# Kernel optimization log

Measured on AMD Instinct MI355X. Metric: run time of the kernel, lower is better.

Reference implementation:

```python
import jax, jax.numpy as jnp
import numpy as np

BATCH = 8192
EXP_DIM = 1024        # experience_dim
DICT_SIZE = 4096      # dictionary_size
SPARSITY = 0.1        # sparsity_level
REG = 0.1             # regularization_strength
STEP = 0.1            # ISTA step size (hardcoded in module)
N_ITERS = 20          # min(max_iterations, 20)
K_SPARSE = int(DICT_SIZE * SPARSITY)  # 409


def setup_inputs() -> dict:
    key = jax.random.key(0)
    k_x, k_dict = jax.random.split(key)
    experiences_batch = jax.random.normal(k_x, (BATCH, EXP_DIM), dtype=jnp.float32)
    # Dictionary init as in __init__: normal*0.1, then row-normalize atoms.
    raw = jax.random.normal(k_dict, (DICT_SIZE, EXP_DIM), dtype=jnp.float32) * 0.1
    atom_norms = jnp.linalg.norm(raw, axis=1, keepdims=True)
    dictionary = raw / (atom_norms + 1e-8)
    return {"experiences_batch": experiences_batch, "dictionary": dictionary}


def reference(experiences_batch, dictionary):
    """Batched ISTA sparse coding (20 steps) + hard top-k sparsification.

    experiences_batch: [B, d]   dictionary: [K, d]   returns alpha: [B, K]
    """
    B = experiences_batch.shape[0]
    K = dictionary.shape[0]
    threshold = REG * STEP
    alpha0 = jnp.zeros((B, K), dtype=experiences_batch.dtype)

    def ista_step(alpha, _):
        # residual = x - D^T alpha  (batched: alpha @ D), grad = -D residual
        residual = experiences_batch - alpha @ dictionary          # [B, d]
        a = alpha + STEP * (residual @ dictionary.T)               # [B, K]
        a = jnp.sign(a) * jnp.maximum(jnp.abs(a) - threshold, 0.0)  # soft threshold
        return a, None

    alpha, _ = jax.lax.scan(ista_step, alpha0, None, length=N_ITERS)

    # Keep only top-k entries by magnitude per row, zero the rest.
    _, idx = jax.lax.top_k(jnp.abs(alpha), K_SPARSE)               # [B, k]
    rows = jnp.arange(B)[:, None]
    sparse_alpha = jnp.zeros_like(alpha).at[rows, idx].set(alpha[rows, idx])
    return sparse_alpha
```

## Files before the change

### kernel.cpp

```cpp
#include <hip/hip_runtime.h>
#include <math.h>

#define BATCH   8192
#define EXP_DIM 1024
#define DICT    4096
#define NIT     20
#define KSP     409
#define STEP_F  0.1f
#define THR_F   0.01f

__device__ __forceinline__ float soft_update(float oldv, float g) {
    float a = oldv + STEP_F * g;
    float m = fabsf(a) - THR_F;
    return m > 0.0f ? copysignf(m, a) : 0.0f;
}

__global__ __launch_bounds__(256)
void transpose_d(const float* __restrict__ D, float* __restrict__ DT) {
    __shared__ float tile[32][33];
    const int t = threadIdx.x;
    const int tx = t & 31, ty = t >> 5;
    const int n0 = blockIdx.x * 32;
    const int k0 = blockIdx.y * 32;
#pragma unroll
    for (int i = 0; i < 4; ++i)
        tile[ty + 8 * i][tx] = D[(size_t)(k0 + ty + 8 * i) * EXP_DIM + n0 + tx];
    __syncthreads();
#pragma unroll
    for (int i = 0; i < 4; ++i)
        DT[(size_t)(n0 + ty + 8 * i) * DICT + k0 + tx] = tile[tx][ty + 8 * i];
}

#define TK 16
#define LDS_LD 132

__global__ __launch_bounds__(256)
void gemm1_nt(const float* __restrict__ Asrc, const float* __restrict__ DT,
              const float* __restrict__ X, float* __restrict__ R) {
    __shared__ float AsT[TK][LDS_LD];
    __shared__ float BsT[TK][LDS_LD];
    const int t  = threadIdx.x;
    const int tx = t & 15, ty = t >> 4;
    const int row0 = blockIdx.y * 128, col0 = blockIdx.x * 128;

    const int arow = t >> 1, akg = (t & 1) << 3;
    const float* pA = Asrc + (size_t)(row0 + arow) * DICT + akg;
    const float* pB = DT   + (size_t)(col0 + arow) * DICT + akg;

    float acc[8][8] = {};

    for (int k0 = 0; k0 < DICT; k0 += TK) {
        float4 a0 = *(const float4*)(pA + k0);
        float4 a1 = *(const float4*)(pA + k0 + 4);
        float4 b0 = *(const float4*)(pB + k0);
        float4 b1 = *(const float4*)(pB + k0 + 4);
        __syncthreads();
        AsT[akg + 0][arow] = a0.x; AsT[akg + 1][arow] = a0.y;
        AsT[akg + 2][arow] = a0.z; AsT[akg + 3][arow] = a0.w;
        AsT[akg + 4][arow] = a1.x; AsT[akg + 5][arow] = a1.y;
        AsT[akg + 6][arow] = a1.z; AsT[akg + 7][arow] = a1.w;
        BsT[akg + 0][arow] = b0.x; BsT[akg + 1][arow] = b0.y;
        BsT[akg + 2][arow] = b0.z; BsT[akg + 3][arow] = b0.w;
        BsT[akg + 4][arow] = b1.x; BsT[akg + 5][arow] = b1.y;
        BsT[akg + 6][arow] = b1.z; BsT[akg + 7][arow] = b1.w;
        __syncthreads();
#pragma unroll
        for (int k = 0; k < TK; ++k) {
            float4 av0 = *(const float4*)&AsT[k][ty * 4];
            float4 av1 = *(const float4*)&AsT[k][64 + ty * 4];
            float4 bv0 = *(const float4*)&BsT[k][tx * 4];
            float4 bv1 = *(const float4*)&BsT[k][64 + tx * 4];
            float av[8] = {av0.x, av0.y, av0.z, av0.w, av1.x, av1.y, av1.z, av1.w};
            float bv[8] = {bv0.x, bv0.y, bv0.z, bv0.w, bv1.x, bv1.y, bv1.z, bv1.w};
#pragma unroll
            for (int i = 0; i < 8; ++i)
#pragma unroll
                for (int j = 0; j < 8; ++j)
                    acc[i][j] += av[i] * bv[j];
        }
    }

#pragma unroll
    for (int i = 0; i < 8; ++i) {
        const int r = row0 + ((i < 4) ? (ty * 4 + i) : (64 + ty * 4 + i - 4));
        {
            const size_t off = (size_t)r * EXP_DIM + col0 + tx * 4;
            float4 xv = *(const float4*)&X[off];
            float4 o;
            o.x = xv.x - acc[i][0]; o.y = xv.y - acc[i][1];
            o.z = xv.z - acc[i][2]; o.w = xv.w - acc[i][3];
            *(float4*)&R[off] = o;
        }
        {
            const size_t off = (size_t)r * EXP_DIM + col0 + 64 + tx * 4;
            float4 xv = *(const float4*)&X[off];
            float4 o;
            o.x = xv.x - acc[i][4]; o.y = xv.y - acc[i][5];
            o.z = xv.z - acc[i][6]; o.w = xv.w - acc[i][7];
            *(float4*)&R[off] = o;
        }
    }
}

__global__ __launch_bounds__(256)
void gemm2_update(const float* __restrict__ Rsrc, const float* __restrict__ D,
                  float* __restrict__ Aa) {
    __shared__ float AsT[TK][LDS_LD];
    __shared__ float BsT[TK][LDS_LD];
    const int t  = threadIdx.x;
    const int tx = t & 15, ty = t >> 4;
    const int row0 = blockIdx.y * 128, col0 = blockIdx.x * 128;

    const int arow = t >> 1, akg = (t & 1) << 3;
    const float* pA = Rsrc + (size_t)(row0 + arow) * EXP_DIM + akg;
    const float* pB = D + (size_t)(col0 + arow) * EXP_DIM + akg;

    float acc[8][8] = {};

    for (int k0 = 0; k0 < EXP_DIM; k0 += TK) {
        float4 a0 = *(const float4*)(pA + k0);
        float4 a1 = *(const float4*)(pA + k0 + 4);
        float4 b0 = *(const float4*)(pB + k0);
        float4 b1 = *(const float4*)(pB + k0 + 4);
        __syncthreads();
        AsT[akg + 0][arow] = a0.x; AsT[akg + 1][arow] = a0.y;
        AsT[akg + 2][arow] = a0.z; AsT[akg + 3][arow] = a0.w;
        AsT[akg + 4][arow] = a1.x; AsT[akg + 5][arow] = a1.y;
        AsT[akg + 6][arow] = a1.z; AsT[akg + 7][arow] = a1.w;
        BsT[akg + 0][arow] = b0.x; BsT[akg + 1][arow] = b0.y;
        BsT[akg + 2][arow] = b0.z; BsT[akg + 3][arow] = b0.w;
        BsT[akg + 4][arow] = b1.x; BsT[akg + 5][arow] = b1.y;
        BsT[akg + 6][arow] = b1.z; BsT[akg + 7][arow] = b1.w;
        __syncthreads();
#pragma unroll
        for (int k = 0; k < TK; ++k) {
            float4 av0 = *(const float4*)&AsT[k][ty * 4];
            float4 av1 = *(const float4*)&AsT[k][64 + ty * 4];
            float4 bv0 = *(const float4*)&BsT[k][tx * 4];
            float4 bv1 = *(const float4*)&BsT[k][64 + tx * 4];
            float av[8] = {av0.x, av0.y, av0.z, av0.w, av1.x, av1.y, av1.z, av1.w};
            float bv[8] = {bv0.x, bv0.y, bv0.z, bv0.w, bv1.x, bv1.y, bv1.z, bv1.w};
#pragma unroll
            for (int i = 0; i < 8; ++i)
#pragma unroll
                for (int j = 0; j < 8; ++j)
                    acc[i][j] += av[i] * bv[j];
        }
    }

#pragma unroll
    for (int i = 0; i < 8; ++i) {
        const int r = row0 + ((i < 4) ? (ty * 4 + i) : (64 + ty * 4 + i - 4));
        {
            float4* p = (float4*)&Aa[(size_t)r * DICT + col0 + tx * 4];
            float4 oldv = *p;
            float4 o;
            o.x = soft_update(oldv.x, acc[i][0]);
            o.y = soft_update(oldv.y, acc[i][1]);
            o.z = soft_update(oldv.z, acc[i][2]);
            o.w = soft_update(oldv.w, acc[i][3]);
            *p = o;
        }
        {
            float4* p = (float4*)&Aa[(size_t)r * DICT + col0 + 64 + tx * 4];
            float4 oldv = *p;
            float4 o;
            o.x = soft_update(oldv.x, acc[i][4]);
            o.y = soft_update(oldv.y, acc[i][5]);
            o.z = soft_update(oldv.z, acc[i][6]);
            o.w = soft_update(oldv.w, acc[i][7]);
            *p = o;
        }
    }
}

#define BM  64
#define BN  64
#define BK  16
#define LDT 68

__global__ __launch_bounds__(256)
void gemm1_resid(const float* __restrict__ A, const float* __restrict__ D,
                 const float* __restrict__ X, float* __restrict__ R) {
    __shared__ float As[BK][LDT];
    __shared__ float Bs[BK][LDT];
    const int t    = threadIdx.x;
    const int row0 = blockIdx.y * BM;
    const int col0 = blockIdx.x * BN;
    const int tx = t & 15, ty = t >> 4;
    const int lr = t >> 2;
    const int lk = (t & 3) << 2;
    const int bkr = t >> 4;
    const int bn  = (t & 15) << 2;

    float acc[4][4] = {};

    for (int k0 = 0; k0 < DICT; k0 += BK) {
        float4 av = *(const float4*)&A[(row0 + lr) * DICT + k0 + lk];
        float4 bv = *(const float4*)&D[(k0 + bkr) * EXP_DIM + col0 + bn];
        __syncthreads();
        As[lk + 0][lr] = av.x; As[lk + 1][lr] = av.y;
        As[lk + 2][lr] = av.z; As[lk + 3][lr] = av.w;
        *(float4*)&Bs[bkr][bn] = bv;
        __syncthreads();
#pragma unroll
        for (int k = 0; k < BK; ++k) {
            float4 a = *(const float4*)&As[k][ty << 2];
            float4 b = *(const float4*)&Bs[k][tx << 2];
            float avr[4] = {a.x, a.y, a.z, a.w};
            float bvr[4] = {b.x, b.y, b.z, b.w};
#pragma unroll
            for (int i = 0; i < 4; ++i)
#pragma unroll
                for (int j = 0; j < 4; ++j)
                    acc[i][j] += avr[i] * bvr[j];
        }
    }

#pragma unroll
    for (int i = 0; i < 4; ++i) {
        int r = row0 + (ty << 2) + i;
        int c = col0 + (tx << 2);
        float4 xv = *(const float4*)&X[r * EXP_DIM + c];
        float4 o;
        o.x = xv.x - acc[i][0];
        o.y = xv.y - acc[i][1];
        o.z = xv.z - acc[i][2];
        o.w = xv.w - acc[i][3];
        *(float4*)&R[r * EXP_DIM + c] = o;
    }
}

__global__ __launch_bounds__(256)
void topk_kernel(float* __restrict__ A) {
    const int row = blockIdx.x;
    float* a = A + (size_t)row * DICT;
    __shared__ unsigned int sb[DICT];
    __shared__ unsigned int hist[256];
    __shared__ unsigned int s_bin, s_need;
    const int t = threadIdx.x;

#pragma unroll
    for (int i = 0; i < DICT / 256; ++i) {
        int j = t + 256 * i;
        sb[j] = __float_as_uint(a[j]) & 0x7fffffffu;
    }

    unsigned int prefix = 0, needed = KSP;
    for (int shift = 24; shift >= 0; shift -= 8) {
        __syncthreads();
        hist[t] = 0;
        __syncthreads();
        unsigned int hmask = (shift == 24) ? 0u : (0xffffffffu << (shift + 8));
        for (int i = 0; i < DICT / 256; ++i) {
            unsigned int b = sb[t + 256 * i];
            if ((b & hmask) == prefix)
                atomicAdd(&hist[(b >> shift) & 0xffu], 1u);
        }
        __syncthreads();
        if (t == 0) {
            unsigned int cum = 0;
            for (int bin = 255; bin >= 0; --bin) {
                unsigned int h = hist[bin];
                if (cum + h >= needed) { s_bin = (unsigned int)bin; s_need = needed - cum; break; }
                cum += h;
            }
        }
        __syncthreads();
        prefix |= s_bin << shift;
        needed = s_need;
    }

    unsigned int E = hist[prefix & 0xffu];
    bool simple = (E == needed) || (prefix == 0);
    if (!simple) {
        if (t == 0) {
            unsigned int cnt = 0;
            for (int j = 0; j < DICT; ++j) {
                if (sb[j] == prefix) {
                    if (cnt < needed) sb[j] |= 0x80000000u;
                    ++cnt;
                }
            }
        }
        __syncthreads();
    }

    for (int i = 0; i < DICT / 256; ++i) {
        int j = t + 256 * i;
        unsigned int b = sb[j];
        bool keep = simple ? (b >= prefix)
                           : (((b & 0x7fffffffu) > prefix) || (b >> 31));
        float v = a[j];
        a[j] = keep ? v : 0.0f;
    }
}

extern "C" void kernel_launch(void* const* d_in, const int* in_sizes, int n_in,
                              void* d_out, int out_size, void* d_ws, size_t ws_size,
                              hipStream_t stream) {
    const float* X = (const float*)d_in[0];
    const float* D = (const float*)d_in[1];
    float* A = (float*)d_out;

    const size_t R_ELEMS  = (size_t)BATCH * EXP_DIM;
    const size_t DT_ELEMS = (size_t)EXP_DIM * DICT;
    const size_t NEED = (R_ELEMS + DT_ELEMS) * sizeof(float);

    hipMemsetAsync(A, 0, (size_t)BATCH * DICT * sizeof(float), stream);

    dim3 blk(256);
    dim3 g2(DICT / 128, BATCH / 128);

    if (ws_size >= NEED) {
        float* R  = (float*)d_ws;
        float* DT = R + R_ELEMS;

        hipLaunchKernelGGL(transpose_d, dim3(EXP_DIM / 32, DICT / 32), blk, 0,
                           stream, D, DT);

        dim3 g1(EXP_DIM / 128, BATCH / 128);
        for (int it = 0; it < NIT; ++it) {
            hipLaunchKernelGGL(gemm1_nt, g1, blk, 0, stream, A, DT, X, R);
            hipLaunchKernelGGL(gemm2_update, g2, blk, 0, stream, R, D, A);
        }
    } else {
        float* R = (float*)d_ws;
        dim3 og1(EXP_DIM / BN, BATCH / BM);
        for (int it = 0; it < NIT; ++it) {
            hipLaunchKernelGGL(gemm1_resid, og1, blk, 0, stream, A, D, X, R);
            hipLaunchKernelGGL(gemm2_update, g2, blk, 0, stream, R, D, A);
        }
    }
    hipLaunchKernelGGL(topk_kernel, dim3(BATCH), blk, 0, stream, A);
}
```

Measured before the change: 30.98 ms.

## Double-buffer LDS tiles in residual GEMM and remap blocks for XCD locality

Gives the gemm1_nt kernel (residual = X - alpha@D) two LDS buffers, so the global loads for the next K-tile are issued before computing on the current tile, leaving one barrier per iteration instead of two. It also remaps the linear block index so that consecutive blocks on the same XCD share row tiles of alpha, aiming for better L2 reuse. The trade-off is doubled LDS use and more live registers, which may lower occupancy. The remap hardcodes an 8x64 grid shape.

```diff
diff --git a/kernel.cpp b/kernel.cpp
--- a/kernel.cpp
+++ b/kernel.cpp
@@ -37,11 +37,15 @@
 __global__ __launch_bounds__(256)
 void gemm1_nt(const float* __restrict__ Asrc, const float* __restrict__ DT,
               const float* __restrict__ X, float* __restrict__ R) {
-    __shared__ float AsT[TK][LDS_LD];
-    __shared__ float BsT[TK][LDS_LD];
+    __shared__ float AsT[2][TK][LDS_LD];
+    __shared__ float BsT[2][TK][LDS_LD];
     const int t  = threadIdx.x;
     const int tx = t & 15, ty = t >> 4;
-    const int row0 = blockIdx.y * 128, col0 = blockIdx.x * 128;
+
+    const int lin = blockIdx.y * 8 + blockIdx.x;
+    const int xcd = lin & 7, j = lin >> 3;
+    const int row0 = ((xcd << 3) | (j >> 3)) * 128;
+    const int col0 = (j & 7) * 128;
 
     const int arow = t >> 1, akg = (t & 1) << 3;
     const float* pA = Asrc + (size_t)(row0 + arow) * DICT + akg;
@@ -49,36 +53,68 @@
 
     float acc[8][8] = {};
 
-    for (int k0 = 0; k0 < DICT; k0 += TK) {
-        float4 a0 = *(const float4*)(pA + k0);
-        float4 a1 = *(const float4*)(pA + k0 + 4);
-        float4 b0 = *(const float4*)(pB + k0);
-        float4 b1 = *(const float4*)(pB + k0 + 4);
-        __syncthreads();
-        AsT[akg + 0][arow] = a0.x; AsT[akg + 1][arow] = a0.y;
-        AsT[akg + 2][arow] = a0.z; AsT[akg + 3][arow] = a0.w;
-        AsT[akg + 4][arow] = a1.x; AsT[akg + 5][arow] = a1.y;
-        AsT[akg + 6][arow] = a1.z; AsT[akg + 7][arow] = a1.w;
-        BsT[akg + 0][arow] = b0.x; BsT[akg + 1][arow] = b0.y;
-        BsT[akg + 2][arow] = b0.z; BsT[akg + 3][arow] = b0.w;
-        BsT[akg + 4][arow] = b1.x; BsT[akg + 5][arow] = b1.y;
-        BsT[akg + 6][arow] = b1.z; BsT[akg + 7][arow] = b1.w;
-        __syncthreads();
-#pragma unroll
-        for (int k = 0; k < TK; ++k) {
-            float4 av0 = *(const float4*)&AsT[k][ty * 4];
-            float4 av1 = *(const float4*)&AsT[k][64 + ty * 4];
-            float4 bv0 = *(const float4*)&BsT[k][tx * 4];
-            float4 bv1 = *(const float4*)&BsT[k][64 + tx * 4];
-            float av[8] = {av0.x, av0.y, av0.z, av0.w, av1.x, av1.y, av1.z, av1.w};
-            float bv[8] = {bv0.x, bv0.y, bv0.z, bv0.w, bv1.x, bv1.y, bv1.z, bv1.w};
-#pragma unroll
-            for (int i = 0; i < 8; ++i)
-#pragma unroll
-                for (int j = 0; j < 8; ++j)
-                    acc[i][j] += av[i] * bv[j];
-        }
-    }
+    {
+        float4 a0 = *(const float4*)(pA);
+        float4 a1 = *(const float4*)(pA + 4);
+        float4 b0 = *(const float4*)(pB);
+        float4 b1 = *(const float4*)(pB + 4);
+        AsT[0][akg + 0][arow] = a0.x; AsT[0][akg + 1][arow] = a0.y;
+        AsT[0][akg + 2][arow] = a0.z; AsT[0][akg + 3][arow] = a0.w;
+        AsT[0][akg + 4][arow] = a1.x; AsT[0][akg + 5][arow] = a1.y;
+        AsT[0][akg + 6][arow] = a1.z; AsT[0][akg + 7][arow] = a1.w;
+        BsT[0][akg + 0][arow] = b0.x; BsT[0][akg + 1][arow] = b0.y;
+        BsT[0][akg + 2][arow] = b0.z; BsT[0][akg + 3][arow] = b0.w;
+        BsT[0][akg + 4][arow] = b1.x; BsT[0][akg + 5][arow] = b1.y;
+        BsT[0][akg + 6][arow] = b1.z; BsT[0][akg + 7][arow] = b1.w;
+    }
+
+    int cur = 0;
+#define G1_COMPUTE(BUF)                                                        \
+    _Pragma("unroll")                                                          \
+    for (int k = 0; k < TK; ++k) {                                             \
+        float4 av0 = *(const float4*)&AsT[BUF][k][ty * 4];                     \
+        float4 av1 = *(const float4*)&AsT[BUF][k][64 + ty * 4];                \
+        float4 bv0 = *(const float4*)&BsT[BUF][k][tx * 4];                     \
+        float4 bv1 = *(const float4*)&BsT[BUF][k][64 + tx * 4];                \
+        float av[8] = {av0.x, av0.y, av0.z, av0.w, av1.x, av1.y, av1.z, av1.w};\
+        float bv[8] = {bv0.x, bv0.y, bv0.z, bv0.w, bv1.x, bv1.y, bv1.z, bv1.w};\
+        _Pragma("unroll")                                                      \
+        for (int i = 0; i < 8; ++i)                                            \
+            _Pragma("unroll")                                                  \
+            for (int jj = 0; jj < 8; ++jj)                                     \
+                acc[i][jj] += av[i] * bv[jj];                                  \
+    }
+
+    for (int t8 = 0; t8 < DICT / TK - 1; ++t8) {
+        __syncthreads();
+        const int kn = (t8 + 1) * TK;
+        float4 na0 = *(const float4*)(pA + kn);
+        float4 na1 = *(const float4*)(pA + kn + 4);
+        float4 nb0 = *(const float4*)(pB + kn);
+        float4 nb1 = *(const float4*)(pB + kn + 4);
+        G1_COMPUTE(cur)
+        const int nx = cur ^ 1;
+        AsT[nx][akg + 0][arow] = na0.x;
+        AsT[nx][akg + 1][arow] = na0.y;
+        AsT[nx][akg + 2][arow] = na0.z;
+        AsT[nx][akg + 3][arow] = na0.w;
+        AsT[nx][akg + 4][arow] = na1.x;
+        AsT[nx][akg + 5][arow] = na1.y;
+        AsT[nx][akg + 6][arow] = na1.z;
+        AsT[nx][akg + 7][arow] = na1.w;
+        BsT[nx][akg + 0][arow] = nb0.x;
+        BsT[nx][akg + 1][arow] = nb0.y;
+        BsT[nx][akg + 2][arow] = nb0.z;
+        BsT[nx][akg + 3][arow] = nb0.w;
+        BsT[nx][akg + 4][arow] = nb1.x;
+        BsT[nx][akg + 5][arow] = nb1.y;
+        BsT[nx][akg + 6][arow] = nb1.z;
+        BsT[nx][akg + 7][arow] = nb1.w;
+        cur = nx;
+    }
+    __syncthreads();
+    G1_COMPUTE(cur)
+#undef G1_COMPUTE
 
 #pragma unroll
     for (int i = 0; i < 8; ++i) {
```

Result: slower. 32.53 ms (+5.0%).
